# Performance work log

Measured on AMD Instinct MI355X. Metric: run time of the kernel, lower is better.

## Reference

```python
import jax, jax.numpy as jnp
import numpy as np

TEMPERATURE = 0.5


def setup_inputs() -> dict:
    key = jax.random.key(0)
    k1, k2 = jax.random.split(key)
    N, D = 4096, 128
    z_i = jax.random.normal(k1, (N, D), dtype=jnp.float32)
    z_j = jax.random.normal(k2, (N, D), dtype=jnp.float32)
    return {"z_i": z_i, "z_j": z_j}


def reference(z_i, z_j):
    # make_permutation interleaves the two views: rows are
    # [z_i[0], z_j[0], z_i[1], z_j[1], ...]  -> shape [2N, D]
    N, D = z_i.shape
    z = jnp.stack([z_i, z_j], axis=1).reshape(2 * N, D)
    # cosine similarity: zTz / (||z_a|| * ||z_b||) == normalized rows matmul
    norm = jnp.linalg.norm(z, axis=-1, keepdims=True)  # [2N, 1]
    s = (z @ z.T) / (norm @ norm.T)                    # [2N, 2N]
    e = jnp.exp(s / TEMPERATURE)
    idx = jnp.arange(2 * N)
    partner = idx ^ 1                                   # (2k <-> 2k+1) positive pairs
    numerator = e[idx, partner]                         # [2N]
    denominator = jnp.sum(e, axis=-1) - jnp.diagonal(e)  # row-sum minus self-sim
    # original sums all 2N per-sample losses then divides by 2N == mean
    return jnp.mean(-jnp.log(numerator / denominator))
```

## Files before the change

kernel.cpp:

```cpp
#include <hip/hip_runtime.h>
#include <hip/hip_bf16.h>

#define N_PAIR 4096
#define N_ROW  8192
#define DIM    128
#define NX     8

typedef __attribute__((ext_vector_type(4))) float f32x4;
typedef __attribute__((ext_vector_type(4))) int   i32x4;
typedef __attribute__((ext_vector_type(8))) int   i32x8;

__device__ inline float fast_exp2(float x) {
#if __has_builtin(__builtin_amdgcn_exp2f)
    return __builtin_amdgcn_exp2f(x);
#else
    float r; asm("v_exp_f32 %0, %1" : "=v"(r) : "v"(x)); return r;
#endif
}
__device__ inline float fast_log2(float x) {
#if __has_builtin(__builtin_amdgcn_logf)
    return __builtin_amdgcn_logf(x);
#else
    float r; asm("v_log_f32 %0, %1" : "=v"(r) : "v"(x)); return r;
#endif
}

__global__ __launch_bounds__(256) void k_prep(const float* __restrict__ zi,
                                              const float* __restrict__ zj,
                                              unsigned char* __restrict__ zh8,
                                              float* __restrict__ pd,
                                              float* __restrict__ rowsum,
                                              float* __restrict__ out) {
    const int wid  = threadIdx.x >> 6;
    const int lane = threadIdx.x & 63;
    const int k    = blockIdx.x * 4 + wid;
    float2 a = *(const float2*)&zi[k * DIM + lane * 2];
    float2 b = *(const float2*)&zj[k * DIM + lane * 2];
    float ssi = a.x * a.x + a.y * a.y;
    float ssj = b.x * b.x + b.y * b.y;
    float dot = a.x * b.x + a.y * b.y;
#pragma unroll
    for (int off = 1; off < 64; off <<= 1) {
        ssi += __shfl_xor(ssi, off);
        ssj += __shfl_xor(ssj, off);
        dot += __shfl_xor(dot, off);
    }
    const float SCL  = 1.6986436816458534f;
    const float invi = rsqrtf(ssi), invj = rsqrtf(ssj);
    const float qi = invi * SCL, qj = invj * SCL;
    unsigned int pi = __builtin_amdgcn_cvt_pk_fp8_f32(a.x * qi, a.y * qi, 0, false);
    unsigned int pj = __builtin_amdgcn_cvt_pk_fp8_f32(b.x * qj, b.y * qj, 0, false);
    ((unsigned short*)zh8)[(2 * k)     * (DIM / 2) + lane] = (unsigned short)pi;
    ((unsigned short*)zh8)[(2 * k + 1) * (DIM / 2) + lane] = (unsigned short)pj;
    if (lane == 0) {
        pd[k] = dot * invi * invj;
        rowsum[2 * k]     = 0.f;
        rowsum[2 * k + 1] = 0.f;
        if (k == 0) out[0] = 0.f;
    }
}

__global__ __launch_bounds__(512, 8) void k_simsum(const unsigned char* __restrict__ zh8,
                                                   float* __restrict__ rowsum) {
    __shared__ unsigned char Bs[2][16384];
    __shared__ float rsum_lds[64];
    const int tid  = threadIdx.x;
    const int lane = tid & 63;
    const int wid  = tid >> 6;
    const int wr   = wid >> 2, wc = wid & 3;
    const int l15  = lane & 15, lhi = lane >> 4;
    const int by   = blockIdx.y;
    const int bx0  = blockIdx.x * NX;
    const int row0 = by * 64 + wr * 32;

    if (tid < 64) rsum_lds[tid] = 0.f;

    i32x8 a[2];
#pragma unroll
    for (int m = 0; m < 2; ++m) {
        const unsigned char* ap = &zh8[(row0 + m * 16 + l15) * DIM + lhi * 32];
        union { i32x4 h[2]; i32x8 v; } u;
        u.h[0] = *(const i32x4*)ap;
        u.h[1] = *(const i32x4*)(ap + 16);
        a[m] = u.v;
    }

    auto stage = [&](int ct, int buf) {
#pragma unroll
        for (int i = 0; i < 2; ++i) {
            const int rl = wr * 16 + i * 8 + (lane >> 3);
            const int g  = (lane & 7) ^ (lane >> 3);
            const unsigned char* src = zh8 + (ct * 128 + wc * 32 + rl) * DIM + g * 16;
            __builtin_amdgcn_global_load_lds(
                (const __attribute__((address_space(1))) void*)src,
                (__attribute__((address_space(3))) void*)(&Bs[buf][wc * 4096 + wr * 2048 + i * 1024]),
                16, 0, 0);
        }
    };

    const int SC1 = 0x7F7F7F7F;
    float rs[2] = {0.f, 0.f};

    stage(bx0, 0);
    asm volatile("s_waitcnt vmcnt(0)" ::: "memory");
    __builtin_amdgcn_s_barrier();

    int cur = 0;
#pragma unroll 1
    for (int t = 0; t < NX; ++t) {
        if (t + 1 < NX) stage(bx0 + t + 1, cur ^ 1);
        const int bx = bx0 + t;
        i32x8 b[2];
#pragma unroll
        for (int n = 0; n < 2; ++n) {
            const int rowb = n * 16 + l15;
            const int base = wc * 4096 + rowb * 128;
            union { i32x4 h[2]; i32x8 v; } u;
            u.h[0] = *(const i32x4*)&Bs[cur][base + (((lhi * 2 + 0) ^ (l15 & 7)) << 4)];
            u.h[1] = *(const i32x4*)&Bs[cur][base + (((lhi * 2 + 1) ^ (l15 & 7)) << 4)];
            b[n] = u.v;
        }
        f32x4 accT[2][2];
        __builtin_amdgcn_s_setprio(1);
#pragma unroll
        for (int n = 0; n < 2; ++n)
#pragma unroll
            for (int m = 0; m < 2; ++m)
                accT[n][m] = __builtin_amdgcn_mfma_scale_f32_16x16x128_f8f6f4(
                    b[n], a[m], (f32x4){0.f, 0.f, 0.f, 0.f},
                    0, 0,
                    0, SC1, 0, SC1);
        __builtin_amdgcn_s_setprio(0);
        if (bx == (by >> 1)) {
            const int coff = (by & 1) * 64;
#pragma unroll
            for (int m = 0; m < 2; ++m) {
                const int rloc = wr * 32 + m * 16 + l15;
                float s0 = 0.f, s1 = 0.f;
#pragma unroll
                for (int n = 0; n < 2; ++n)
#pragma unroll
                    for (int r = 0; r < 4; ++r) {
                        const int cloc = wc * 32 + n * 16 + lhi * 4 + r;
                        float v = fast_exp2(accT[n][m][r]);
                        v = (cloc == coff + rloc) ? 0.f : v;
                        if (n == 0) s0 += v; else s1 += v;
                    }
                rs[m] += s0 + s1;
            }
        } else {
#pragma unroll
            for (int m = 0; m < 2; ++m) {
                float s0 = 0.f, s1 = 0.f;
#pragma unroll
                for (int n = 0; n < 2; ++n)
#pragma unroll
                    for (int r = 0; r < 4; ++r) {
                        float v = fast_exp2(accT[n][m][r]);
                        if (n == 0) s0 += v; else s1 += v;
                    }
                rs[m] += s0 + s1;
            }
        }
        if (t + 1 < NX) {
            asm volatile("s_waitcnt vmcnt(0)" ::: "memory");
            __builtin_amdgcn_s_barrier();
            cur ^= 1;
        }
    }

#pragma unroll
    for (int m = 0; m < 2; ++m) {
        rs[m] += __shfl_xor(rs[m], 16);
        rs[m] += __shfl_xor(rs[m], 32);
    }
    __syncthreads();
    if (lane < 16) {
#pragma unroll
        for (int m = 0; m < 2; ++m)
            atomicAdd(&rsum_lds[wr * 32 + m * 16 + lane], rs[m]);
    }
    __syncthreads();
    if (tid < 64) atomicAdd(&rowsum[by * 64 + tid], rsum_lds[tid]);
}

__global__ __launch_bounds__(256) void k_loss(const float* __restrict__ rowsum,
                                              const float* __restrict__ pd,
                                              float* __restrict__ out) {
    const int tid  = threadIdx.x;
    const int lane = tid & 63;
    const int wid  = tid >> 6;
    const int i    = blockIdx.x * 256 + tid;
    const float LN2 = 0.6931471805599453f;
    float local = fast_log2(rowsum[i]) * LN2 - 2.f * pd[i >> 1];
#pragma unroll
    for (int off = 1; off < 64; off <<= 1) local += __shfl_xor(local, off);
    __shared__ float wsum[4];
    if (lane == 0) wsum[wid] = local;
    __syncthreads();
    if (tid == 0)
        atomicAdd(out, (wsum[0] + wsum[1] + wsum[2] + wsum[3]) * (1.f / (float)N_ROW));
}

extern "C" void kernel_launch(void* const* d_in, const int* in_sizes, int n_in,
                              void* d_out, int out_size, void* d_ws, size_t ws_size,
                              hipStream_t stream) {
    const float* zi = (const float*)d_in[0];
    const float* zj = (const float*)d_in[1];
    char* ws = (char*)d_ws;
    unsigned char* zh8 = (unsigned char*)ws;
    float* rowsum = (float*)(ws + 2 * 1024 * 1024);
    float* pd     = (float*)(ws + 2 * 1024 * 1024 + 32 * 1024);

    k_prep<<<N_PAIR / 4, 256, 0, stream>>>(zi, zj, zh8, pd, rowsum, (float*)d_out);
    dim3 grid(64 / NX, 128);
    k_simsum<<<grid, 512, 0, stream>>>(zh8, rowsum);
    k_loss<<<N_ROW / 256, 256, 0, stream>>>(rowsum, pd, (float*)d_out);
}
```

Measured before the change: 28.85 us.

## Give each wave a private LDS tile to drop per-iteration block barriers

Each wave now stages and reads its own 4 KB slice of B in LDS, so the B tile is no longer shared across the block. The double buffer and the per-iteration block-wide s_barrier are replaced by per-wave waitcnt ordering: the wave reads its fragment, waits on lgkmcnt, then issues the next global_load_lds into the same slice. This removes barrier stalls between waves, at the cost of duplicate global loads (wr pairs of waves now both fetch the same 32 columns) and of losing the overlap between the next prefetch and the current LDS read.

```diff
diff --git a/kernel.cpp b/kernel.cpp
--- a/kernel.cpp
+++ b/kernel.cpp
@@ -62,7 +62,7 @@
 
 __global__ __launch_bounds__(512, 8) void k_simsum(const unsigned char* __restrict__ zh8,
                                                    float* __restrict__ rowsum) {
-    __shared__ unsigned char Bs[2][16384];
+    __shared__ unsigned char Bs[8 * 4096];
     __shared__ float rsum_lds[64];
     const int tid  = threadIdx.x;
     const int lane = tid & 63;
@@ -72,8 +72,10 @@
     const int by   = blockIdx.y;
     const int bx0  = blockIdx.x * NX;
     const int row0 = by * 64 + wr * 32;
+    const int wbase = wid * 4096;
 
     if (tid < 64) rsum_lds[tid] = 0.f;
+    __syncthreads();
 
     i32x8 a[2];
 #pragma unroll
@@ -85,15 +87,24 @@
         a[m] = u.v;
     }
 
-    auto stage = [&](int ct, int buf) {
-#pragma unroll
-        for (int i = 0; i < 2; ++i) {
-            const int rl = wr * 16 + i * 8 + (lane >> 3);
-            const int g  = (lane & 7) ^ (lane >> 3);
-            const unsigned char* src = zh8 + (ct * 128 + wc * 32 + rl) * DIM + g * 16;
+    const int rl      = lane >> 3;
+    const int stg_off = (wc * 32 + rl) * DIM + (((lane & 7) ^ (rl & 7)) << 4);
+    int rd_off[2][2];
+#pragma unroll
+    for (int n = 0; n < 2; ++n) {
+        const int rowb = n * 16 + l15;
+#pragma unroll
+        for (int c = 0; c < 2; ++c)
+            rd_off[n][c] = wbase + rowb * 128 + (((lhi * 2 + c) ^ (l15 & 7)) << 4);
+    }
+
+    auto stage = [&](int ct) {
+#pragma unroll
+        for (int i = 0; i < 4; ++i) {
+            const unsigned char* src = zh8 + ct * (128 * DIM) + stg_off + i * (8 * DIM);
             __builtin_amdgcn_global_load_lds(
                 (const __attribute__((address_space(1))) void*)src,
-                (__attribute__((address_space(3))) void*)(&Bs[buf][wc * 4096 + wr * 2048 + i * 1024]),
+                (__attribute__((address_space(3))) void*)(&Bs[wbase + i * 1024]),
                 16, 0, 0);
         }
     };
@@ -101,25 +112,23 @@
     const int SC1 = 0x7F7F7F7F;
     float rs[2] = {0.f, 0.f};
 
-    stage(bx0, 0);
+    stage(bx0);
     asm volatile("s_waitcnt vmcnt(0)" ::: "memory");
-    __builtin_amdgcn_s_barrier();
-
-    int cur = 0;
+
 #pragma unroll 1
     for (int t = 0; t < NX; ++t) {
-        if (t + 1 < NX) stage(bx0 + t + 1, cur ^ 1);
         const int bx = bx0 + t;
         i32x8 b[2];
 #pragma unroll
         for (int n = 0; n < 2; ++n) {
-            const int rowb = n * 16 + l15;
-            const int base = wc * 4096 + rowb * 128;
             union { i32x4 h[2]; i32x8 v; } u;
-            u.h[0] = *(const i32x4*)&Bs[cur][base + (((lhi * 2 + 0) ^ (l15 & 7)) << 4)];
-            u.h[1] = *(const i32x4*)&Bs[cur][base + (((lhi * 2 + 1) ^ (l15 & 7)) << 4)];
+            u.h[0] = *(const i32x4*)&Bs[rd_off[n][0]];
+            u.h[1] = *(const i32x4*)&Bs[rd_off[n][1]];
             b[n] = u.v;
         }
+        asm volatile("s_waitcnt lgkmcnt(0)" ::: "memory");
+        if (t + 1 < NX) stage(bx0 + t + 1);
+
         f32x4 accT[2][2];
         __builtin_amdgcn_s_setprio(1);
 #pragma unroll
@@ -131,6 +140,7 @@
                     0, 0,
                     0, SC1, 0, SC1);
         __builtin_amdgcn_s_setprio(0);
+
         if (bx == (by >> 1)) {
             const int coff = (by & 1) * 64;
 #pragma unroll
@@ -162,11 +172,8 @@
                 rs[m] += s0 + s1;
             }
         }
-        if (t + 1 < NX) {
+        if (t + 1 < NX)
             asm volatile("s_waitcnt vmcnt(0)" ::: "memory");
-            __builtin_amdgcn_s_barrier();
-            cur ^= 1;
-        }
     }
 
 #pragma unroll
@@ -174,7 +181,6 @@
         rs[m] += __shfl_xor(rs[m], 16);
         rs[m] += __shfl_xor(rs[m], 32);
     }
-    __syncthreads();
     if (lane < 16) {
 #pragma unroll
         for (int m = 0; m < 2; ++m)
```

After: 28.18 us, median of 2. 1.02x faster.
